# Kernel tuning notes

Hardware: AMD Instinct MI355X
Metric: run time of the kernel (lower is better)

## Reference

```python
import jax, jax.numpy as jnp
import numpy as np

N_HEADS = 16

def setup_inputs() -> dict:
    key = jax.random.key(0)
    k1, k2, k3 = jax.random.split(key, 3)
    B, T, C = 2, 2048, 1024
    x = jax.random.normal(k1, (B, T, C), dtype=jnp.float32)
    W_qkv = jax.random.normal(k2, (3 * C, C), dtype=jnp.float32) * 0.02
    b_qkv = jnp.zeros((3 * C,), dtype=jnp.float32)
    W_proj = jax.random.normal(k3, (C, C), dtype=jnp.float32) * 0.02
    b_proj = jnp.zeros((C,), dtype=jnp.float32)
    return {"x": x, "W_qkv": W_qkv, "b_qkv": b_qkv, "W_proj": W_proj, "b_proj": b_proj}

def reference(x, W_qkv, b_qkv, W_proj, b_proj):
    B, T, C = x.shape
    H = N_HEADS
    hd = C // H
    # fused QKV projection: (B,T,3C)
    qkv = x @ W_qkv.T + b_qkv
    # mirror torch: reshape to (B,T,H,3*hd) then chunk along last dim
    qkv = qkv.reshape(B, T, H, 3 * hd)
    q, k, v = jnp.split(qkv, 3, axis=-1)  # each (B,T,H,hd)
    q = q / jnp.sqrt(jnp.asarray(hd, dtype=q.dtype))
    # scaled dot-product attention, non-causal, full matrix (faithful to source)
    att = jnp.einsum('bihd,bjhd->bhij', q, k)  # (B,H,T,T)
    att = jax.nn.softmax(att, axis=-1)
    out = jnp.einsum('bhij,bjhd->bihd', att, v)  # (B,T,H,hd)
    out = out.reshape(B, T, C)
    return out @ W_proj.T + b_proj
```

## Files before the change

kernel.cpp:

```cpp
#include <hip/hip_runtime.h>


typedef __bf16 bf16x4 __attribute__((ext_vector_type(4)));
typedef __bf16 bf16x8 __attribute__((ext_vector_type(8)));
typedef float  f32x4  __attribute__((ext_vector_type(4)));

#define AS1(p) ((const __attribute__((address_space(1))) void*)(p))
#define AS3(p) ((__attribute__((address_space(3))) void*)(p))

__global__ __launch_bounds__(256)
void cvt_all(const float* __restrict__ a, const float* __restrict__ b,
             const float* __restrict__ c, __bf16* __restrict__ oa,
             __bf16* __restrict__ ob, __bf16* __restrict__ oc,
             int na, int nb, int nc)
{
    const int total = (na + nb + nc) >> 2;
    const int stride = gridDim.x * blockDim.x;
    for (int i4 = blockIdx.x * blockDim.x + threadIdx.x; i4 < total; i4 += stride) {
        int i = i4 << 2;
        const float* src; __bf16* dst;
        if (i < na)               { src = a + i;             dst = oa + i; }
        else if (i < na + nb)     { src = b + (i - na);      dst = ob + (i - na); }
        else                      { src = c + (i - na - nb); dst = oc + (i - na - nb); }
        const float4 v = *(const float4*)src;
        bf16x4 o = { (__bf16)v.x, (__bf16)v.y, (__bf16)v.z, (__bf16)v.w };
        *(bf16x4*)dst = o;
    }
}

template<int MODE>
__global__ __launch_bounds__(256)
void gemm_bt(const __bf16* __restrict__ A, const __bf16* __restrict__ W,
             const float* __restrict__ bias, int M, int N, int K,
             __bf16* __restrict__ O0, __bf16* __restrict__ O1,
             __bf16* __restrict__ O2, float* __restrict__ Of)
{
    __shared__ __bf16 sA[128 * 64];
    __shared__ __bf16 sB[128 * 64];
    const int tid  = threadIdx.x;
    const int w    = tid >> 6, lane = tid & 63;
    const int g    = lane >> 4, r16 = lane & 15;
    const int lin  = blockIdx.y * gridDim.x + blockIdx.x;
    const int per  = (gridDim.x * gridDim.y) >> 3;
    const int nlin = (lin & 7) * per + (lin >> 3);
    const int tM   = (nlin / gridDim.x) * 128, tN = (nlin % gridDim.x) * 128;
    const int wr   = w >> 1, wc = w & 1;
    const int crow = lane >> 3;
    const int ccol = (lane & 7) * 8;

    f32x4 acc[4][4] = {};

    for (int k0 = 0; k0 < K; k0 += 64) {
#pragma unroll
        for (int c = w; c < 16; c += 4) {
            const __bf16* ga = A + (size_t)(tM + c * 8 + crow) * K + k0 + ccol;
            __builtin_amdgcn_global_load_lds(AS1(ga), AS3(&sA[c * 8 * 64]), 16, 0, 0);
            const __bf16* gb = W + (size_t)(tN + c * 8 + crow) * K + k0 + ccol;
            __builtin_amdgcn_global_load_lds(AS1(gb), AS3(&sB[c * 8 * 64]), 16, 0, 0);
        }
        __syncthreads();
#pragma unroll
        for (int kk = 0; kk < 2; ++kk) {
            bf16x8 a[4], b[4];
#pragma unroll
            for (int mf = 0; mf < 4; ++mf)
                a[mf] = *(const bf16x8*)&sA[(wr * 64 + mf * 16 + r16) * 64 + kk * 32 + g * 8];
#pragma unroll
            for (int nf = 0; nf < 4; ++nf)
                b[nf] = *(const bf16x8*)&sB[(wc * 64 + nf * 16 + r16) * 64 + kk * 32 + g * 8];
#pragma unroll
            for (int mf = 0; mf < 4; ++mf)
#pragma unroll
                for (int nf = 0; nf < 4; ++nf)
                    acc[mf][nf] = __builtin_amdgcn_mfma_f32_16x16x32_bf16(
                        a[mf], b[nf], acc[mf][nf], 0, 0, 0);
        }
        __syncthreads();
    }

#pragma unroll
    for (int mf = 0; mf < 4; ++mf) {
#pragma unroll
        for (int nf = 0; nf < 4; ++nf) {
#pragma unroll
            for (int reg = 0; reg < 4; ++reg) {
                const int row = tM + wr * 64 + mf * 16 + g * 4 + reg;
                const int col = tN + wc * 64 + nf * 16 + r16;
                float v = acc[mf][nf][reg] + bias[col];
                if (MODE == 0) {
                    const int h = col / 192, j = col % 192;
                    const int b = row >> 11, t = row & 2047;
                    const size_t bh = (size_t)(b * 16 + h);
                    if (j < 64)
                        O0[(bh * 2048 + t) * 64 + j] = (__bf16)(v * 0.18033688011112042f);
                    else if (j < 128)
                        O1[(bh * 2048 + t) * 64 + (j - 64)] = (__bf16)v;
                    else
                        O2[(bh * 64 + (j - 128)) * 2048 + t] = (__bf16)v;
                } else {
                    Of[(size_t)row * N + col] = v;
                }
            }
        }
    }
}

__global__ __launch_bounds__(256, 2)
void attn(const __bf16* __restrict__ Q, const __bf16* __restrict__ K,
          const __bf16* __restrict__ V, __bf16* __restrict__ O)
{
    __shared__ __bf16 sK[2][64 * 64];
    __shared__ __bf16 sV[2][64 * 64];

    const int tid = threadIdx.x;
    const int w   = tid >> 6, lane = tid & 63;
    const int g   = lane >> 4, r16 = lane & 15;
    const int m      = blockIdx.x;
    const int within = m >> 3;
    const int bh     = (m & 7) + ((within >> 4) << 3);
    const int qb     = within & 15;
    const int q0     = qb * 128 + w * 32;
    const __bf16* Qp = Q + (size_t)bh * 2048 * 64;
    const __bf16* Kp = K + (size_t)bh * 2048 * 64;
    const __bf16* Vp = V + (size_t)bh * 64 * 2048;

    const int srow  = lane >> 3;
    const int scolV = 8 * ((lane & 7) ^ srow);
    const int scolK = 8 * ((lane & 7) ^ ((srow & 3) | ((w & 1) << 2)));
    const int swzK  = ((r16 & 3) | (((r16 >> 2) & 1) << 2)) << 4;
    const int swzV  = (r16 & 7) << 4;

    bf16x8 qa[2][2];
#pragma unroll
    for (int h = 0; h < 2; ++h)
#pragma unroll
        for (int kk = 0; kk < 2; ++kk)
            qa[h][kk] = *(const bf16x8*)(Qp + (size_t)(q0 + h * 16 + r16) * 64 + kk * 32 + g * 8);

    f32x4 o[2][4] = {};
    float mrun[2] = { -1e30f, -1e30f }, lrun[2] = { 0.f, 0.f };

#pragma unroll
    for (int r = 0; r < 2; ++r) {
        const int ldsb = r * 4096 + w * 1024;
        const int row  = r * 32 + w * 8 + srow;
        __builtin_amdgcn_global_load_lds(AS1(Kp + (size_t)row * 64 + scolK),
                                         AS3((char*)&sK[0][0] + ldsb), 16, 0, 0);
        __builtin_amdgcn_global_load_lds(AS1(Vp + (size_t)row * 2048 + scolV),
                                         AS3((char*)&sV[0][0] + ldsb), 16, 0, 0);
    }
    __syncthreads();

    for (int t = 0; t < 32; ++t) {
        const int cur = t & 1;
        if (t < 31) {
            const int kvn = (t + 1) * 64;
#pragma unroll
            for (int r = 0; r < 2; ++r) {
                const int ldsb = r * 4096 + w * 1024;
                const int row  = r * 32 + w * 8 + srow;
                __builtin_amdgcn_global_load_lds(AS1(Kp + (size_t)(kvn + row) * 64 + scolK),
                                                 AS3((char*)&sK[cur ^ 1][0] + ldsb), 16, 0, 0);
                __builtin_amdgcn_global_load_lds(AS1(Vp + (size_t)row * 2048 + kvn + scolV),
                                                 AS3((char*)&sV[cur ^ 1][0] + ldsb), 16, 0, 0);
            }
        }
        bf16x8 kb[4][2];
#pragma unroll
        for (int nf = 0; nf < 4; ++nf) {
            const int row = ((nf >> 1) << 5) + ((r16 >> 2) << 3) + ((nf & 1) << 2) + (r16 & 3);
#pragma unroll
            for (int kk = 0; kk < 2; ++kk)
                kb[nf][kk] = *(const bf16x8*)((const char*)&sK[cur][0] + row * 128
                                              + ((kk * 64 + g * 16) ^ swzK));
        }
        f32x4 S[2][4];
        __builtin_amdgcn_s_setprio(1);
#pragma unroll
        for (int h = 0; h < 2; ++h)
#pragma unroll
            for (int nf = 0; nf < 4; ++nf) {
                f32x4 s = {};
                s = __builtin_amdgcn_mfma_f32_16x16x32_bf16(kb[nf][0], qa[h][0], s, 0, 0, 0);
                s = __builtin_amdgcn_mfma_f32_16x16x32_bf16(kb[nf][1], qa[h][1], s, 0, 0, 0);
                S[h][nf] = s;
            }
        __builtin_amdgcn_s_setprio(0);
        float rm[2];
#pragma unroll
        for (int h = 0; h < 2; ++h) {
            float m0 = fmaxf(fmaxf(S[h][0][0], S[h][0][1]), fmaxf(S[h][0][2], S[h][0][3]));
#pragma unroll
            for (int nf = 1; nf < 4; ++nf)
                m0 = fmaxf(m0, fmaxf(fmaxf(S[h][nf][0], S[h][nf][1]),
                                     fmaxf(S[h][nf][2], S[h][nf][3])));
            m0 = fmaxf(m0, __shfl_xor(m0, 16));
            m0 = fmaxf(m0, __shfl_xor(m0, 32));
            rm[h] = m0;
        }
        if (!__all(rm[0] <= mrun[0] + 8.f && rm[1] <= mrun[1] + 8.f)) {
#pragma unroll
            for (int h = 0; h < 2; ++h) {
                const float mn = fmaxf(mrun[h], rm[h]);
                const float al = exp2f(mrun[h] - mn);
#pragma unroll
                for (int df = 0; df < 4; ++df)
#pragma unroll
                    for (int reg = 0; reg < 4; ++reg) o[h][df][reg] *= al;
                lrun[h] *= al;
                mrun[h] = mn;
            }
        }
        bf16x8 pb[2][2];
#pragma unroll
        for (int h = 0; h < 2; ++h) {
            float ps = 0.f;
#pragma unroll
            for (int nf = 0; nf < 4; ++nf)
#pragma unroll
                for (int reg = 0; reg < 4; ++reg) {
                    const float p = exp2f(S[h][nf][reg] - mrun[h]);
                    S[h][nf][reg] = p;
                    ps += p;
                }
            lrun[h] += ps;
#pragma unroll
            for (int kk = 0; kk < 2; ++kk) {
                bf16x8 tpk;
                tpk[0] = (__bf16)S[h][kk * 2][0];     tpk[1] = (__bf16)S[h][kk * 2][1];
                tpk[2] = (__bf16)S[h][kk * 2][2];     tpk[3] = (__bf16)S[h][kk * 2][3];
                tpk[4] = (__bf16)S[h][kk * 2 + 1][0]; tpk[5] = (__bf16)S[h][kk * 2 + 1][1];
                tpk[6] = (__bf16)S[h][kk * 2 + 1][2]; tpk[7] = (__bf16)S[h][kk * 2 + 1][3];
                pb[h][kk] = tpk;
            }
        }
        __builtin_amdgcn_s_setprio(1);
#pragma unroll
        for (int kk = 0; kk < 2; ++kk)
#pragma unroll
            for (int df = 0; df < 4; ++df) {
                const int row = df * 16 + r16;
                bf16x8 vb = *(const bf16x8*)((const char*)&sV[cur][0] + row * 128
                                             + ((kk * 64 + g * 16) ^ swzV));
#pragma unroll
                for (int h = 0; h < 2; ++h)
                    o[h][df] = __builtin_amdgcn_mfma_f32_16x16x32_bf16(vb, pb[h][kk], o[h][df], 0, 0, 0);
            }
        __builtin_amdgcn_s_setprio(0);
        __syncthreads();
    }

#pragma unroll
    for (int h = 0; h < 2; ++h) {
        float l = lrun[h];
        l += __shfl_xor(l, 16);
        l += __shfl_xor(l, 32);
        const float inv = 1.f / l;
        const size_t token = (size_t)(bh >> 4) * 2048 + q0 + h * 16 + r16;
#pragma unroll
        for (int df = 0; df < 4; ++df) {
            bf16x4 ov = { (__bf16)(o[h][df][0] * inv), (__bf16)(o[h][df][1] * inv),
                          (__bf16)(o[h][df][2] * inv), (__bf16)(o[h][df][3] * inv) };
            *(bf16x4*)(O + token * 1024 + (bh & 15) * 64 + df * 16 + g * 4) = ov;
        }
    }
}

extern "C" void kernel_launch(void* const* d_in, const int* in_sizes, int n_in,
                              void* d_out, int out_size, void* d_ws, size_t ws_size,
                              hipStream_t stream)
{
    const float* x     = (const float*)d_in[0];
    const float* Wqkv  = (const float*)d_in[1];
    const float* bqkv  = (const float*)d_in[2];
    const float* Wproj = (const float*)d_in[3];
    const float* bproj = (const float*)d_in[4];
    float* out = (float*)d_out;

    const size_t NX   = (size_t)4096 * 1024;
    const size_t NWQ  = (size_t)3072 * 1024;
    const size_t NWP  = (size_t)1024 * 1024;

    __bf16* xb  = (__bf16*)d_ws;
    __bf16* Wqb = xb  + NX;
    __bf16* Wpb = Wqb + NWQ;
    __bf16* Qs  = Wpb + NWP;
    __bf16* Ks  = Qs  + NX;
    __bf16* Vt  = Ks  + NX;
    __bf16* Os  = Vt  + NX;

    cvt_all<<<dim3(2048), dim3(256), 0, stream>>>(x, Wqkv, Wproj, xb, Wqb, Wpb,
                                                  (int)NX, (int)NWQ, (int)NWP);
    gemm_bt<0><<<dim3(24, 32), dim3(256), 0, stream>>>(xb, Wqb, bqkv, 4096, 3072, 1024, Qs, Ks, Vt, nullptr);
    attn<<<dim3(512), dim3(256), 0, stream>>>(Qs, Ks, Vt, Os);
    gemm_bt<1><<<dim3(8, 32), dim3(256), 0, stream>>>(Os, Wpb, bproj, 4096, 1024, 1024, nullptr, nullptr, nullptr, out);
}
```

Before: 147.0 us.

## Halve attention block size, fold max into MFMA init, MFMA row-sum, vectorize V stores

The attention kernel drops to 2 waves per block (64 queries) on a 3D grid of 1024 blocks, with each wave loading 4 K/V rows per stage from precomputed pointers. The running max is subtracted by seeding the QK MFMA accumulator with -m, so the rescale path and its cross-lane shuffles run only when the new max exceeds it by more than 8. Row sums come from an MFMA against a ones vector, and exp2 uses the raw hardware builtin. Separately, the QKV GEMM epilogue writes the transposed V with packed 4-wide bf16 stores. Together these cut VALU and shuffle work and raise occupancy, in exchange for more blocks, more redundant K/V traffic, and bf16-rounded sums in the normalizer.

```diff
diff --git a/kernel.cpp b/kernel.cpp
--- a/kernel.cpp
+++ b/kernel.cpp
@@ -82,30 +82,41 @@
     for (int mf = 0; mf < 4; ++mf) {
 #pragma unroll
         for (int nf = 0; nf < 4; ++nf) {
-#pragma unroll
-            for (int reg = 0; reg < 4; ++reg) {
-                const int row = tM + wr * 64 + mf * 16 + g * 4 + reg;
-                const int col = tN + wc * 64 + nf * 16 + r16;
-                float v = acc[mf][nf][reg] + bias[col];
-                if (MODE == 0) {
-                    const int h = col / 192, j = col % 192;
-                    const int b = row >> 11, t = row & 2047;
-                    const size_t bh = (size_t)(b * 16 + h);
-                    if (j < 64)
-                        O0[(bh * 2048 + t) * 64 + j] = (__bf16)(v * 0.18033688011112042f);
-                    else if (j < 128)
-                        O1[(bh * 2048 + t) * 64 + (j - 64)] = (__bf16)v;
-                    else
-                        O2[(bh * 64 + (j - 128)) * 2048 + t] = (__bf16)v;
+            if (MODE == 0) {
+                const int col  = tN + wc * 64 + nf * 16 + r16;
+                const int h    = col / 192, j = col % 192;
+                const int rowb = tM + wr * 64 + mf * 16 + g * 4;
+                const int b    = rowb >> 11, t = rowb & 2047;
+                const size_t bh = (size_t)(b * 16 + h);
+                const float bs = bias[col];
+                if (j >= 128) {
+                    bf16x4 pk = { (__bf16)(acc[mf][nf][0] + bs), (__bf16)(acc[mf][nf][1] + bs),
+                                  (__bf16)(acc[mf][nf][2] + bs), (__bf16)(acc[mf][nf][3] + bs) };
+                    *(bf16x4*)&O2[(bh * 64 + (j - 128)) * 2048 + t] = pk;
+                } else if (j < 64) {
+#pragma unroll
+                    for (int reg = 0; reg < 4; ++reg)
+                        O0[(bh * 2048 + t + reg) * 64 + j] =
+                            (__bf16)((acc[mf][nf][reg] + bs) * 0.18033688011112042f);
                 } else {
-                    Of[(size_t)row * N + col] = v;
+#pragma unroll
+                    for (int reg = 0; reg < 4; ++reg)
+                        O1[(bh * 2048 + t + reg) * 64 + (j - 64)] =
+                            (__bf16)(acc[mf][nf][reg] + bs);
                 }
+            } else {
+#pragma unroll
+                for (int reg = 0; reg < 4; ++reg) {
+                    const int row = tM + wr * 64 + mf * 16 + g * 4 + reg;
+                    const int col = tN + wc * 64 + nf * 16 + r16;
+                    Of[(size_t)row * N + col] = acc[mf][nf][reg] + bias[col];
+                }
             }
         }
     }
 }
 
-__global__ __launch_bounds__(256, 2)
+__global__ __launch_bounds__(128, 2)
 void attn(const __bf16* __restrict__ Q, const __bf16* __restrict__ K,
           const __bf16* __restrict__ V, __bf16* __restrict__ O)
 {
@@ -115,18 +126,18 @@
     const int tid = threadIdx.x;
     const int w   = tid >> 6, lane = tid & 63;
     const int g   = lane >> 4, r16 = lane & 15;
-    const int m      = blockIdx.x;
-    const int within = m >> 3;
-    const int bh     = (m & 7) + ((within >> 4) << 3);
-    const int qb     = within & 15;
-    const int q0     = qb * 128 + w * 32;
+    const int m   = blockIdx.x + (blockIdx.y << 5) + (blockIdx.z << 9);
+    const int bh  = (m & 7) + ((m >> 8) << 3);
+    const int qb  = (m >> 3) & 31;
+    const int q0  = qb * 64 + w * 32;
     const __bf16* Qp = Q + (size_t)bh * 2048 * 64;
     const __bf16* Kp = K + (size_t)bh * 2048 * 64;
     const __bf16* Vp = V + (size_t)bh * 64 * 2048;
 
     const int srow  = lane >> 3;
     const int scolV = 8 * ((lane & 7) ^ srow);
-    const int scolK = 8 * ((lane & 7) ^ ((srow & 3) | ((w & 1) << 2)));
+    const int scolK0 = 8 * ((lane & 7) ^ (srow & 3));
+    const int scolK1 = 8 * ((lane & 7) ^ ((srow & 3) | 4));
     const int swzK  = ((r16 & 3) | (((r16 >> 2) & 1) << 2)) << 4;
     const int swzV  = (r16 & 7) << 4;
 
@@ -137,32 +148,41 @@
         for (int kk = 0; kk < 2; ++kk)
             qa[h][kk] = *(const bf16x8*)(Qp + (size_t)(q0 + h * 16 + r16) * 64 + kk * 32 + g * 8);
 
+    bf16x8 ones;
+#pragma unroll
+    for (int i = 0; i < 8; ++i) ones[i] = (__bf16)1.0f;
+
     f32x4 o[2][4] = {};
-    float mrun[2] = { -1e30f, -1e30f }, lrun[2] = { 0.f, 0.f };
-
-#pragma unroll
-    for (int r = 0; r < 2; ++r) {
-        const int ldsb = r * 4096 + w * 1024;
-        const int row  = r * 32 + w * 8 + srow;
-        __builtin_amdgcn_global_load_lds(AS1(Kp + (size_t)row * 64 + scolK),
-                                         AS3((char*)&sK[0][0] + ldsb), 16, 0, 0);
-        __builtin_amdgcn_global_load_lds(AS1(Vp + (size_t)row * 2048 + scolV),
-                                         AS3((char*)&sV[0][0] + ldsb), 16, 0, 0);
+    f32x4 lsum[2] = {};
+    float mrun[2] = { 0.f, 0.f };
+
+    const char* kp[4]; const char* vp[4]; int ldsb[4];
+#pragma unroll
+    for (int r = 0; r < 4; ++r) {
+        const int row = w * 32 + r * 8 + srow;
+        kp[r]   = (const char*)(Kp + (size_t)row * 64 + ((r & 1) ? scolK1 : scolK0));
+        vp[r]   = (const char*)(Vp + (size_t)row * 2048 + scolV);
+        ldsb[r] = w * 4096 + r * 1024;
+    }
+
+#pragma unroll
+    for (int r = 0; r < 4; ++r) {
+        __builtin_amdgcn_global_load_lds(AS1(kp[r]), AS3((char*)&sK[0][0] + ldsb[r]), 16, 0, 0);
+        __builtin_amdgcn_global_load_lds(AS1(vp[r]), AS3((char*)&sV[0][0] + ldsb[r]), 16, 0, 0);
+        kp[r] += 8192; vp[r] += 128;
     }
     __syncthreads();
 
     for (int t = 0; t < 32; ++t) {
         const int cur = t & 1;
         if (t < 31) {
-            const int kvn = (t + 1) * 64;
-#pragma unroll
-            for (int r = 0; r < 2; ++r) {
-                const int ldsb = r * 4096 + w * 1024;
-                const int row  = r * 32 + w * 8 + srow;
-                __builtin_amdgcn_global_load_lds(AS1(Kp + (size_t)(kvn + row) * 64 + scolK),
-                                                 AS3((char*)&sK[cur ^ 1][0] + ldsb), 16, 0, 0);
-                __builtin_amdgcn_global_load_lds(AS1(Vp + (size_t)row * 2048 + kvn + scolV),
-                                                 AS3((char*)&sV[cur ^ 1][0] + ldsb), 16, 0, 0);
+            char* const kd = (char*)&sK[cur ^ 1][0];
+            char* const vd = (char*)&sV[cur ^ 1][0];
+#pragma unroll
+            for (int r = 0; r < 4; ++r) {
+                __builtin_amdgcn_global_load_lds(AS1(kp[r]), AS3(kd + ldsb[r]), 16, 0, 0);
+                __builtin_amdgcn_global_load_lds(AS1(vp[r]), AS3(vd + ldsb[r]), 16, 0, 0);
+                kp[r] += 8192; vp[r] += 128;
             }
         }
         bf16x8 kb[4][2];
@@ -177,14 +197,14 @@
         f32x4 S[2][4];
         __builtin_amdgcn_s_setprio(1);
 #pragma unroll
-        for (int h = 0; h < 2; ++h)
+        for (int h = 0; h < 2; ++h) {
+            const f32x4 cinit = { -mrun[h], -mrun[h], -mrun[h], -mrun[h] };
 #pragma unroll
             for (int nf = 0; nf < 4; ++nf) {
-                f32x4 s = {};
-                s = __builtin_amdgcn_mfma_f32_16x16x32_bf16(kb[nf][0], qa[h][0], s, 0, 0, 0);
-                s = __builtin_amdgcn_mfma_f32_16x16x32_bf16(kb[nf][1], qa[h][1], s, 0, 0, 0);
-                S[h][nf] = s;
-            }
+                f32x4 s = __builtin_amdgcn_mfma_f32_16x16x32_bf16(kb[nf][0], qa[h][0], cinit, 0, 0, 0);
+                S[h][nf] = __builtin_amdgcn_mfma_f32_16x16x32_bf16(kb[nf][1], qa[h][1], s, 0, 0, 0);
+            }
+        }
         __builtin_amdgcn_s_setprio(0);
         float rm[2];
 #pragma unroll
@@ -194,47 +214,51 @@
             for (int nf = 1; nf < 4; ++nf)
                 m0 = fmaxf(m0, fmaxf(fmaxf(S[h][nf][0], S[h][nf][1]),
                                      fmaxf(S[h][nf][2], S[h][nf][3])));
-            m0 = fmaxf(m0, __shfl_xor(m0, 16));
-            m0 = fmaxf(m0, __shfl_xor(m0, 32));
             rm[h] = m0;
         }
-        if (!__all(rm[0] <= mrun[0] + 8.f && rm[1] <= mrun[1] + 8.f)) {
+        if (!__all(rm[0] <= 8.f && rm[1] <= 8.f)) {
 #pragma unroll
             for (int h = 0; h < 2; ++h) {
-                const float mn = fmaxf(mrun[h], rm[h]);
-                const float al = exp2f(mrun[h] - mn);
+                float r0 = rm[h];
+                r0 = fmaxf(r0, __shfl_xor(r0, 16));
+                r0 = fmaxf(r0, __shfl_xor(r0, 32));
+                const float delta = fmaxf(r0, 0.f);
+                const float al = __builtin_amdgcn_exp2f(-delta);
 #pragma unroll
                 for (int df = 0; df < 4; ++df)
 #pragma unroll
                     for (int reg = 0; reg < 4; ++reg) o[h][df][reg] *= al;
-                lrun[h] *= al;
-                mrun[h] = mn;
+#pragma unroll
+                for (int reg = 0; reg < 4; ++reg) lsum[h][reg] *= al;
+                mrun[h] += delta;
+#pragma unroll
+                for (int nf = 0; nf < 4; ++nf)
+#pragma unroll
+                    for (int reg = 0; reg < 4; ++reg) S[h][nf][reg] -= delta;
             }
         }
         bf16x8 pb[2][2];
 #pragma unroll
-        for (int h = 0; h < 2; ++h) {
-            float ps = 0.f;
-#pragma unroll
-            for (int nf = 0; nf < 4; ++nf)
-#pragma unroll
-                for (int reg = 0; reg < 4; ++reg) {
-                    const float p = exp2f(S[h][nf][reg] - mrun[h]);
-                    S[h][nf][reg] = p;
-                    ps += p;
-                }
-            lrun[h] += ps;
+        for (int h = 0; h < 2; ++h)
 #pragma unroll
             for (int kk = 0; kk < 2; ++kk) {
                 bf16x8 tpk;
-                tpk[0] = (__bf16)S[h][kk * 2][0];     tpk[1] = (__bf16)S[h][kk * 2][1];
-                tpk[2] = (__bf16)S[h][kk * 2][2];     tpk[3] = (__bf16)S[h][kk * 2][3];
-                tpk[4] = (__bf16)S[h][kk * 2 + 1][0]; tpk[5] = (__bf16)S[h][kk * 2 + 1][1];
-                tpk[6] = (__bf16)S[h][kk * 2 + 1][2]; tpk[7] = (__bf16)S[h][kk * 2 + 1][3];
+                tpk[0] = (__bf16)__builtin_amdgcn_exp2f(S[h][kk * 2][0]);
+                tpk[1] = (__bf16)__builtin_amdgcn_exp2f(S[h][kk * 2][1]);
+                tpk[2] = (__bf16)__builtin_amdgcn_exp2f(S[h][kk * 2][2]);
+                tpk[3] = (__bf16)__builtin_amdgcn_exp2f(S[h][kk * 2][3]);
+                tpk[4] = (__bf16)__builtin_amdgcn_exp2f(S[h][kk * 2 + 1][0]);
+                tpk[5] = (__bf16)__builtin_amdgcn_exp2f(S[h][kk * 2 + 1][1]);
+                tpk[6] = (__bf16)__builtin_amdgcn_exp2f(S[h][kk * 2 + 1][2]);
+                tpk[7] = (__bf16)__builtin_amdgcn_exp2f(S[h][kk * 2 + 1][3]);
                 pb[h][kk] = tpk;
             }
-        }
         __builtin_amdgcn_s_setprio(1);
+#pragma unroll
+        for (int h = 0; h < 2; ++h) {
+            lsum[h] = __builtin_amdgcn_mfma_f32_16x16x32_bf16(ones, pb[h][0], lsum[h], 0, 0, 0);
+            lsum[h] = __builtin_amdgcn_mfma_f32_16x16x32_bf16(ones, pb[h][1], lsum[h], 0, 0, 0);
+        }
 #pragma unroll
         for (int kk = 0; kk < 2; ++kk)
 #pragma unroll
@@ -252,10 +276,7 @@
 
 #pragma unroll
     for (int h = 0; h < 2; ++h) {
-        float l = lrun[h];
-        l += __shfl_xor(l, 16);
-        l += __shfl_xor(l, 32);
-        const float inv = 1.f / l;
+        const float inv = 1.f / lsum[h][0];
         const size_t token = (size_t)(bh >> 4) * 2048 + q0 + h * 16 + r16;
 #pragma unroll
         for (int df = 0; df < 4; ++df) {
@@ -292,6 +313,6 @@
     cvt_all<<<dim3(2048), dim3(256), 0, stream>>>(x, Wqkv, Wproj, xb, Wqb, Wpb,
                                                   (int)NX, (int)NWQ, (int)NWP);
     gemm_bt<0><<<dim3(24, 32), dim3(256), 0, stream>>>(xb, Wqb, bqkv, 4096, 3072, 1024, Qs, Ks, Vt, nullptr);
-    attn<<<dim3(512), dim3(256), 0, stream>>>(Qs, Ks, Vt, Os);
+    attn<<<dim3(32, 16, 2), dim3(128), 0, stream>>>(Qs, Ks, Vt, Os);
     gemm_bt<1><<<dim3(8, 32), dim3(256), 0, stream>>>(Os, Wpb, bproj, 4096, 1024, 1024, nullptr, nullptr, nullptr, out);
 }
```

Result: faster. 119.5 us (-18.7%).
